# Kernel optimization log

Hardware: AMD Instinct MI355X
Metric: run time of the kernel (lower is better)

## Reference

```python
import jax, jax.numpy as jnp
import numpy as np

T, B, H, L = 512, 64, 512, 2  # seq len, batch, hidden (=input_size), num_layers


def setup_inputs() -> dict:
    key = jax.random.key(0)
    ks = jax.random.split(key, 8)
    s = 1.0 / np.sqrt(H)  # PyTorch LSTMCell init scale
    return {
        "x": jax.random.normal(ks[0], (T, B, H), dtype=jnp.float32),
        "hx": jax.random.normal(ks[1], (L, B, H), dtype=jnp.float32),
        "cx": jax.random.normal(ks[2], (L, B, H), dtype=jnp.float32),
        "W_ih": jax.random.uniform(ks[3], (L, 4 * H, H), jnp.float32, -s, s),
        "W_hh": jax.random.uniform(ks[4], (L, 4 * H, H), jnp.float32, -s, s),
        "b_ih": jax.random.uniform(ks[5], (L, 4 * H), jnp.float32, -s, s),
        "b_hh": jax.random.uniform(ks[6], (L, 4 * H), jnp.float32, -s, s),
    }


def _lstm_cell(x, h, c, W_ih, W_hh, b_ih, b_hh):
    # gates: [B, 4H], PyTorch gate order i, f, g, o
    gates = x @ W_ih.T + b_ih + h @ W_hh.T + b_hh
    i, f, g, o = jnp.split(gates, 4, axis=-1)
    c_new = jax.nn.sigmoid(f) * c + jax.nn.sigmoid(i) * jnp.tanh(g)
    h_new = jax.nn.sigmoid(o) * jnp.tanh(c_new)
    return h_new, c_new


def reference(x, hx, cx, W_ih, W_hh, b_ih, b_hh):
    num_layers = W_ih.shape[0]

    def step(carry, x_t):
        hs, cs = carry  # each [L, B, H]
        inp = x_t
        new_h, new_c = [], []
        for l in range(num_layers):
            h, c = _lstm_cell(inp, hs[l], cs[l], W_ih[l], W_hh[l], b_ih[l], b_hh[l])
            new_h.append(h)
            new_c.append(c)
            inp = h  # feed current-timestep output to next layer (matches torch code)
        return (jnp.stack(new_h), jnp.stack(new_c)), inp

    (hx_f, cx_f), output = jax.lax.scan(step, (hx, cx), x)
    return output, (hx_f, cx_f)
```

## Files before the change

kernel.cpp:

```cpp
#include <hip/hip_runtime.h>
#include <hip/hip_bf16.h>
#include <stdint.h>

#define Tn 512
#define Bn 64
#define Hn 512
#define LDP 520
#define NWG 128
#define NTHR 512
#define BnHn (Bn * Hn)

typedef unsigned short u16;
typedef unsigned int u32;
typedef unsigned long long u64;
typedef __attribute__((ext_vector_type(8))) short bf16x8;
typedef __attribute__((ext_vector_type(4))) float f32x4;

#define HIST_OFF 16384

__device__ __forceinline__ u16 f2bf(float f) {
  u32 u = __float_as_uint(f);
  u = (u + 0x7FFFu + ((u >> 16) & 1u)) >> 16;
  return (u16)u;
}
__device__ __forceinline__ float sigf(float x) { return 1.f / (1.f + __expf(-x)); }
__device__ __forceinline__ float mytanh(float x) {
  float e = __expf(2.f * x);
  return 1.f - 2.f / (e + 1.f);
}
__device__ __forceinline__ u32 ald32(const u32* p) {
  return __hip_atomic_load(p, __ATOMIC_RELAXED, __HIP_MEMORY_SCOPE_AGENT);
}

extern "C" __global__ void __launch_bounds__(256)
lstm_prep(const float* __restrict__ x, const float* __restrict__ hx,
          u32* __restrict__ ws, int xok, int histok) {
  u16* hist = (u16*)((char*)ws + HIST_OFF);
  u16* xbf  = hist + (size_t)(histok ? 513 : 8) * 2 * BnHn;
  const int slot_init = histok ? 512 : 7;
  const int gt = blockIdx.x * 256 + threadIdx.x;
  if (xok) {
#pragma unroll
    for (int i = 0; i < 8; ++i) {
      const int c = gt + (i << 19);
      const float4 v = *(const float4*)(x + (size_t)c * 4);
      const u64 pk = (u64)((u32)f2bf(v.x) | ((u32)f2bf(v.y) << 16)) |
                     ((u64)((u32)f2bf(v.z) | ((u32)f2bf(v.w) << 16)) << 32);
      *(u64*)(xbf + (size_t)c * 4) = pk;
    }
  }
  if (gt < 32768) {
    const int e0 = 2 * gt;
    const int l = e0 >> 15;
    const int off = e0 & 32767;
    const u32 pk = (u32)f2bf(hx[e0]) | ((u32)f2bf(hx[e0 + 1]) << 16);
    *(u32*)(hist + ((size_t)slot_init * 2 + l) * BnHn + off) = pk;
  }
}

extern "C" __global__ void __launch_bounds__(NTHR, 2)
lstm_fused(const float* __restrict__ x, const float* __restrict__ hx,
           const float* __restrict__ cx, const float* __restrict__ Wih,
           const float* __restrict__ Whh, const float* __restrict__ bih,
           const float* __restrict__ bhh, float* __restrict__ out,
           u32* __restrict__ ws, int xok, int histok) {
  __shared__ u16 sh_inp[32 * LDP];
  __shared__ u16 sh_h[32 * LDP];

  __builtin_amdgcn_fence(__ATOMIC_ACQUIRE, "agent");

  const int wg = blockIdx.x;
  const int tid = threadIdx.x;
  const int layer = wg >> 6;
  const int rem = wg & 63;
  const int shalf = rem >> 5;
  const int cc = rem & 31;
  const int wave = tid >> 6;
  const int lane = tid & 63;
  const int l15 = lane & 15;
  const int lhi = lane >> 4;
  const int mt = wave >> 1;
  const int nt = wave & 1;

  u32* flags = ws;
  u16* hist  = (u16*)((char*)ws + HIST_OFF);
  u16* xbf   = hist + (size_t)(histok ? 513 : 8) * 2 * BnHn;
  const int init_slot = histok ? 512 : 7;
  const int gid = layer * 2 + shalf;

  const int jrow = mt * 16 + l15;
  const int gateA = jrow & 3, colA = jrow >> 2;
  const int growA = gateA * Hn + cc * 16 + colA;
  const float* wihp = Wih + ((size_t)layer * 4 * Hn + growA) * Hn;
  const float* whhp = Whh + ((size_t)layer * 4 * Hn + growA) * Hn;
  bf16x8 wih_f[16], whh_f[16];
#pragma unroll
  for (int kt = 0; kt < 16; ++kt) {
    const int k0 = kt * 32 + lhi * 8;
    const float4 va0 = *(const float4*)(wihp + k0);
    const float4 va1 = *(const float4*)(wihp + k0 + 4);
    const float4 vb0 = *(const float4*)(whhp + k0);
    const float4 vb1 = *(const float4*)(whhp + k0 + 4);
    bf16x8 a, b;
    a[0]=(short)f2bf(va0.x); a[1]=(short)f2bf(va0.y); a[2]=(short)f2bf(va0.z); a[3]=(short)f2bf(va0.w);
    a[4]=(short)f2bf(va1.x); a[5]=(short)f2bf(va1.y); a[6]=(short)f2bf(va1.z); a[7]=(short)f2bf(va1.w);
    b[0]=(short)f2bf(vb0.x); b[1]=(short)f2bf(vb0.y); b[2]=(short)f2bf(vb0.z); b[3]=(short)f2bf(vb0.w);
    b[4]=(short)f2bf(vb1.x); b[5]=(short)f2bf(vb1.y); b[6]=(short)f2bf(vb1.z); b[7]=(short)f2bf(vb1.w);
    wih_f[kt] = a; whh_f[kt] = b;
  }

  const int colE = cc * 16 + mt * 4 + lhi;
  const int sampE = shalf * 32 + nt * 16 + l15;
  float bias[4];
#pragma unroll
  for (int r = 0; r < 4; ++r) {
    const int grow = r * Hn + cc * 16 + mt * 4 + lhi;
    bias[r] = bih[layer * 4 * Hn + grow] + bhh[layer * 4 * Hn + grow];
  }
  float c_cur = cx[((size_t)layer * Bn + sampE) * Hn + colE];

  int pidx, tgtoff;
  if (layer == 0) {
    if (lane < 32) { pidx = (0 * 2 + shalf) * 32 + lane; tgtoff = 0; }
    else if (histok) { pidx = (0 * 2 + shalf) * 32 + (lane - 32); tgtoff = 0; }
    else { pidx = (1 * 2 + shalf) * 32 + (lane - 32); tgtoff = 1; }
  } else {
    if (lane < 32) { pidx = (1 * 2 + shalf) * 32 + lane; tgtoff = 0; }
    else { pidx = (0 * 2 + shalf) * 32 + (lane - 32); tgtoff = 1; }
  }
  const u32* pollp = &flags[pidx];

  auto stage_x = [&](int t) {
    if (xok) {
      const u16* ip = xbf + ((size_t)t * Bn + shalf * 32) * Hn;
#pragma unroll
      for (int i = 0; i < 4; ++i) {
        const int chunk = tid + i * 512;
        const int row = chunk >> 6, c0 = (chunk & 63) * 8;
        const uint4 v = *(const uint4*)(ip + (size_t)row * Hn + c0);
        *(uint4*)(&sh_inp[row * LDP + c0]) = v;
      }
    } else {
      const float* xp = x + ((size_t)t * Bn + shalf * 32) * Hn;
#pragma unroll
      for (int i = 0; i < 8; ++i) {
        const int chunk = tid + i * 512;
        const int row = chunk >> 7, c0 = (chunk & 127) * 4;
        const float4 v = *(const float4*)(xp + (size_t)row * Hn + c0);
        const u32 p0 = (u32)f2bf(v.x) | ((u32)f2bf(v.y) << 16);
        const u32 p1 = (u32)f2bf(v.z) | ((u32)f2bf(v.w) << 16);
        *(uint2*)(&sh_inp[row * LDP + c0]) = make_uint2(p0, p1);
      }
    }
  };
  auto stage_h = [&](int slot, int srclayer, u16* dst) {
    const u16* hp = hist + ((size_t)slot * 2 + srclayer) * BnHn + (size_t)(shalf * 32) * Hn;
    if (histok) {
#pragma unroll
      for (int i = 0; i < 4; ++i) {
        const int chunk = tid + i * 512;
        const int row = chunk >> 6, c0 = (chunk & 63) * 8;
        const uint4 v = *(const uint4*)(hp + (size_t)row * Hn + c0);
        *(uint4*)(&dst[row * LDP + c0]) = v;
      }
    } else {
#pragma unroll
      for (int i = 0; i < 8; ++i) {
        const int chunk = tid + i * 512;
        const int row = chunk >> 7, c0 = (chunk & 127) * 4;
        const u64 v = __hip_atomic_load((const u64*)(hp + (size_t)row * Hn + c0),
                                        __ATOMIC_RELAXED, __HIP_MEMORY_SCOPE_AGENT);
        *(u64*)(&dst[row * LDP + c0]) = v;
      }
    }
  };
  f32x4 aI0 = {0.f,0.f,0.f,0.f}, aI1 = {0.f,0.f,0.f,0.f};
  auto compute_aI = [&]() {
    f32x4 t0 = {0.f,0.f,0.f,0.f}, t1 = {0.f,0.f,0.f,0.f};
    const int brow = (nt * 16 + l15) * LDP;
#pragma unroll
    for (int kt = 0; kt < 16; kt += 2) {
      const bf16x8 bi0 = *(const bf16x8*)(&sh_inp[brow + kt * 32 + lhi * 8]);
      const bf16x8 bi1 = *(const bf16x8*)(&sh_inp[brow + (kt + 1) * 32 + lhi * 8]);
      t0 = __builtin_amdgcn_mfma_f32_16x16x32_bf16(wih_f[kt], bi0, t0, 0, 0, 0);
      t1 = __builtin_amdgcn_mfma_f32_16x16x32_bf16(wih_f[kt + 1], bi1, t1, 0, 0, 0);
    }
    aI0 = t0; aI1 = t1;
  };

  if (layer == 0) stage_x(0);
  __syncthreads();
  if (layer == 0) compute_aI();

  const int smax = Tn + 2;
  u32 ep = 0;
  for (int s = 0; s <= smax; ++s) {
    const int t = layer ? s - 3 : s;
    const bool act = (t >= 0) && (t < Tn);

    if (act) {
      const int slotR = (t == 0) ? init_slot : (histok ? (t - 1) : ((t - 1) & 7));
      stage_h(slotR, layer, sh_h);
    }
    __syncthreads();

    float hn = 0.f, cn = 0.f;
    if (act) {
      f32x4 b0 = {0,0,0,0}, b1 = {0,0,0,0};
      const int brow = (nt * 16 + l15) * LDP;
#pragma unroll
      for (int kt = 0; kt < 16; kt += 2) {
        const bf16x8 bh0 = *(const bf16x8*)(&sh_h[brow + kt * 32 + lhi * 8]);
        const bf16x8 bh1 = *(const bf16x8*)(&sh_h[brow + (kt + 1) * 32 + lhi * 8]);
        b0 = __builtin_amdgcn_mfma_f32_16x16x32_bf16(whh_f[kt], bh0, b0, 0, 0, 0);
        b1 = __builtin_amdgcn_mfma_f32_16x16x32_bf16(whh_f[kt + 1], bh1, b1, 0, 0, 0);
      }
      const float gi = aI0[0] + aI1[0] + b0[0] + b1[0] + bias[0];
      const float gf = aI0[1] + aI1[1] + b0[1] + b1[1] + bias[1];
      const float gg = aI0[2] + aI1[2] + b0[2] + b1[2] + bias[2];
      const float go_ = aI0[3] + aI1[3] + b0[3] + b1[3] + bias[3];
      cn = sigf(gf) * c_cur + sigf(gi) * mytanh(gg);
      hn = sigf(go_) * mytanh(cn);
      c_cur = cn;

      const u32 hu = (u32)f2bf(hn);
      const u32 pair = hu | (__shfl_xor(hu, 16) << 16);
      const u32 hi2 = __shfl_xor(pair, 32);
      if (lhi == 0) {
        const int slotW = histok ? t : (t & 7);
        const u64 v8 = (u64)pair | ((u64)hi2 << 32);
        u16* wp = hist + ((size_t)slotW * 2 + layer) * BnHn + (size_t)sampE * Hn + cc * 16 + mt * 4;
        __hip_atomic_store((u64*)wp, v8, __ATOMIC_RELAXED, __HIP_MEMORY_SCOPE_AGENT);
      }
    }
    asm volatile("s_waitcnt vmcnt(0)" ::: "memory");
    __syncthreads();
    ++ep;
    if (tid == 0)
      __hip_atomic_store(&flags[gid * 32 + cc], ep,
                         __ATOMIC_RELAXED, __HIP_MEMORY_SCOPE_AGENT);

    if (act) {
      if (layer == 1)
        out[((size_t)t * Bn + sampE) * Hn + colE] = hn;
      if (t == Tn - 1) {
        out[(size_t)Tn * Bn * Hn + ((size_t)layer * Bn + sampE) * Hn + colE] = hn;
        out[(size_t)Tn * Bn * Hn + (size_t)2 * Bn * Hn + ((size_t)layer * Bn + sampE) * Hn + colE] = cn;
      }
    }
    bool ihnext = false;
    if (layer == 0) {
      if (s + 1 < Tn) { stage_x(s + 1); ihnext = true; }
    } else {
      const int u = s - 2;
      if (u >= 0 && u < Tn) {
        const int slotI = histok ? u : (u & 7);
        stage_h(slotI, 0, sh_inp);
        ihnext = true;
      }
    }
    __syncthreads();
    if (ihnext) compute_aI();

    if (s == smax) break;

    while (true) {
      const u32 v = ald32(pollp);
      if (__all((int)(v + (u32)tgtoff >= ep))) break;
    }
    asm volatile("" ::: "memory");
  }
}

extern "C" void kernel_launch(void* const* d_in, const int* in_sizes, int n_in,
                              void* d_out, int out_size, void* d_ws, size_t ws_size,
                              hipStream_t stream) {
  const float* x   = (const float*)d_in[0];
  const float* hx  = (const float*)d_in[1];
  const float* cx  = (const float*)d_in[2];
  const float* Wih = (const float*)d_in[3];
  const float* Whh = (const float*)d_in[4];
  const float* bih = (const float*)d_in[5];
  const float* bhh = (const float*)d_in[6];
  float* outp = (float*)d_out;
  u32* wsp = (u32*)d_ws;

  const size_t slot_bytes = (size_t)2 * Bn * Hn * 2;
  int histok = (ws_size >= HIST_OFF + (size_t)513 * slot_bytes) ? 1 : 0;
  const size_t xoff = HIST_OFF + (size_t)(histok ? 513 : 8) * slot_bytes;
  int xok = (ws_size >= xoff + (size_t)Tn * Bn * Hn * 2) ? 1 : 0;

  hipMemsetAsync(d_ws, 0, HIST_OFF, stream);

  lstm_prep<<<dim3(2048), dim3(256), 0, stream>>>(x, hx, wsp, xok, histok);

  void* args[] = {(void*)&x, (void*)&hx, (void*)&cx, (void*)&Wih, (void*)&Whh,
                  (void*)&bih, (void*)&bhh, (void*)&outp, (void*)&wsp,
                  (void*)&xok, (void*)&histok};
  hipError_t e = hipLaunchCooperativeKernel((const void*)lstm_fused, dim3(NWG),
                                            dim3(NTHR), args, 0, stream);
  if (e != hipSuccess) {
    lstm_fused<<<dim3(NWG), dim3(NTHR), 0, stream>>>(x, hx, cx, Wih, Whh, bih, bhh,
                                                     outp, wsp, xok, histok);
  }
}
```

Measured before the change: 1.748 ms.

## Replace flag polling with per-element stamped history for LSTM cross-workgroup sync

Adds a stamped mode in which each hidden-state pair is written as a 64-bit word carrying a timestep stamp. Readers spin on the stamps of exactly the data they need instead of waiting on per-workgroup flags, which removes the vmcnt drain, the extra barrier and the flag round-trip on every step. The cost is a history buffer twice as large (about 134MB) that must be memset each call, plus more memory traffic. Launch bounds also drop occupancy from 2 workgroups per CU to 1.

```diff
diff --git a/kernel.cpp b/kernel.cpp
--- a/kernel.cpp
+++ b/kernel.cpp
@@ -17,6 +17,7 @@
 typedef __attribute__((ext_vector_type(4))) float f32x4;
 
 #define HIST_OFF 16384
+#define STAMP_BYTES 134479872ULL
 
 __device__ __forceinline__ u16 f2bf(float f) {
   u32 u = __float_as_uint(f);
@@ -31,13 +32,17 @@
 __device__ __forceinline__ u32 ald32(const u32* p) {
   return __hip_atomic_load(p, __ATOMIC_RELAXED, __HIP_MEMORY_SCOPE_AGENT);
 }
+__device__ __forceinline__ u64 ald64(const u64* p) {
+  return __hip_atomic_load(p, __ATOMIC_RELAXED, __HIP_MEMORY_SCOPE_AGENT);
+}
 
 extern "C" __global__ void __launch_bounds__(256)
 lstm_prep(const float* __restrict__ x, const float* __restrict__ hx,
-          u32* __restrict__ ws, int xok, int histok) {
+          u32* __restrict__ ws, int xok, int smode, int histok) {
   u16* hist = (u16*)((char*)ws + HIST_OFF);
-  u16* xbf  = hist + (size_t)(histok ? 513 : 8) * 2 * BnHn;
-  const int slot_init = histok ? 512 : 7;
+  u64* hstamp = (u64*)((char*)ws + HIST_OFF);
+  u16* xbf = smode ? (u16*)((char*)ws + HIST_OFF + STAMP_BYTES)
+                   : hist + (size_t)(histok ? 513 : 8) * 2 * BnHn;
   const int gt = blockIdx.x * 256 + threadIdx.x;
   if (xok) {
 #pragma unroll
@@ -54,16 +59,24 @@
     const int l = e0 >> 15;
     const int off = e0 & 32767;
     const u32 pk = (u32)f2bf(hx[e0]) | ((u32)f2bf(hx[e0 + 1]) << 16);
-    *(u32*)(hist + ((size_t)slot_init * 2 + l) * BnHn + off) = pk;
-  }
-}
-
-extern "C" __global__ void __launch_bounds__(NTHR, 2)
+    if (smode) {
+      const int b = off >> 9;
+      const int unit = (off & 511) >> 1;
+      hstamp[((size_t)512 * 2 + l) * 16384 + (size_t)b * 256 + unit] =
+          (u64)pk | (15ULL << 32);
+    } else {
+      const int slot_init = histok ? 512 : 7;
+      *(u32*)(hist + ((size_t)slot_init * 2 + l) * BnHn + off) = pk;
+    }
+  }
+}
+
+extern "C" __global__ void __launch_bounds__(NTHR, 1)
 lstm_fused(const float* __restrict__ x, const float* __restrict__ hx,
            const float* __restrict__ cx, const float* __restrict__ Wih,
            const float* __restrict__ Whh, const float* __restrict__ bih,
            const float* __restrict__ bhh, float* __restrict__ out,
-           u32* __restrict__ ws, int xok, int histok) {
+           u32* __restrict__ ws, int xok, int smode, int histok) {
   __shared__ u16 sh_inp[32 * LDP];
   __shared__ u16 sh_h[32 * LDP];
 
@@ -84,7 +97,9 @@
 
   u32* flags = ws;
   u16* hist  = (u16*)((char*)ws + HIST_OFF);
-  u16* xbf   = hist + (size_t)(histok ? 513 : 8) * 2 * BnHn;
+  u64* hstamp = (u64*)((char*)ws + HIST_OFF);
+  u16* xbf = smode ? (u16*)((char*)ws + HIST_OFF + STAMP_BYTES)
+                   : hist + (size_t)(histok ? 513 : 8) * 2 * BnHn;
   const int init_slot = histok ? 512 : 7;
   const int gid = layer * 2 + shalf;
 
@@ -119,6 +134,146 @@
   }
   float c_cur = cx[((size_t)layer * Bn + sampE) * Hn + colE];
 
+  auto stage_x = [&](int t) {
+    if (xok) {
+      const u16* ip = xbf + ((size_t)t * Bn + shalf * 32) * Hn;
+#pragma unroll
+      for (int i = 0; i < 4; ++i) {
+        const int chunk = tid + i * 512;
+        const int row = chunk >> 6, c0 = (chunk & 63) * 8;
+        const uint4 v = *(const uint4*)(ip + (size_t)row * Hn + c0);
+        *(uint4*)(&sh_inp[row * LDP + c0]) = v;
+      }
+    } else {
+      const float* xp = x + ((size_t)t * Bn + shalf * 32) * Hn;
+#pragma unroll
+      for (int i = 0; i < 8; ++i) {
+        const int chunk = tid + i * 512;
+        const int row = chunk >> 7, c0 = (chunk & 127) * 4;
+        const float4 v = *(const float4*)(xp + (size_t)row * Hn + c0);
+        const u32 p0 = (u32)f2bf(v.x) | ((u32)f2bf(v.y) << 16);
+        const u32 p1 = (u32)f2bf(v.z) | ((u32)f2bf(v.w) << 16);
+        *(uint2*)(&sh_inp[row * LDP + c0]) = make_uint2(p0, p1);
+      }
+    }
+  };
+  f32x4 aI0 = {0.f,0.f,0.f,0.f}, aI1 = {0.f,0.f,0.f,0.f};
+  auto compute_aI = [&]() {
+    f32x4 t0 = {0.f,0.f,0.f,0.f}, t1 = {0.f,0.f,0.f,0.f};
+    const int brow = (nt * 16 + l15) * LDP;
+#pragma unroll
+    for (int kt = 0; kt < 16; kt += 2) {
+      const bf16x8 bi0 = *(const bf16x8*)(&sh_inp[brow + kt * 32 + lhi * 8]);
+      const bf16x8 bi1 = *(const bf16x8*)(&sh_inp[brow + (kt + 1) * 32 + lhi * 8]);
+      t0 = __builtin_amdgcn_mfma_f32_16x16x32_bf16(wih_f[kt], bi0, t0, 0, 0, 0);
+      t1 = __builtin_amdgcn_mfma_f32_16x16x32_bf16(wih_f[kt + 1], bi1, t1, 0, 0, 0);
+    }
+    aI0 = t0; aI1 = t1;
+  };
+  auto do_compute = [&](int t, float& hn, float& cn) {
+    f32x4 b0 = {0,0,0,0}, b1 = {0,0,0,0};
+    const int brow = (nt * 16 + l15) * LDP;
+#pragma unroll
+    for (int kt = 0; kt < 16; kt += 2) {
+      const bf16x8 bh0 = *(const bf16x8*)(&sh_h[brow + kt * 32 + lhi * 8]);
+      const bf16x8 bh1 = *(const bf16x8*)(&sh_h[brow + (kt + 1) * 32 + lhi * 8]);
+      b0 = __builtin_amdgcn_mfma_f32_16x16x32_bf16(whh_f[kt], bh0, b0, 0, 0, 0);
+      b1 = __builtin_amdgcn_mfma_f32_16x16x32_bf16(whh_f[kt + 1], bh1, b1, 0, 0, 0);
+    }
+    const float gi = aI0[0] + aI1[0] + b0[0] + b1[0] + bias[0];
+    const float gf = aI0[1] + aI1[1] + b0[1] + b1[1] + bias[1];
+    const float gg = aI0[2] + aI1[2] + b0[2] + b1[2] + bias[2];
+    const float go_ = aI0[3] + aI1[3] + b0[3] + b1[3] + bias[3];
+    cn = sigf(gf) * c_cur + sigf(gi) * mytanh(gg);
+    hn = sigf(go_) * mytanh(cn);
+    c_cur = cn;
+  };
+
+  if (smode) {
+    auto stage_stamped = [&](int slot, int srclayer, u32 expect, u16* dst) {
+      u64* base = hstamp + ((size_t)slot * 2 + srclayer) * 16384 + (size_t)(shalf * 32) * 256;
+#pragma unroll
+      for (int i = 0; i < 8; ++i) {
+        const int p = tid + i * 512;
+        const int samp = p >> 7, up = p & 127;
+        const u64* a = base + samp * 256 + 2 * up;
+        uint4 v = *(const uint4*)a;
+        if (v.y != expect || v.w != expect) {
+          u64 q0, q1;
+          do { q0 = ald64(a); } while ((u32)(q0 >> 32) != expect);
+          do { q1 = ald64(a + 1); } while ((u32)(q1 >> 32) != expect);
+          v.x = (u32)q0; v.z = (u32)q1;
+        }
+        *(uint2*)(&dst[samp * LDP + 4 * up]) = make_uint2(v.x, v.z);
+      }
+    };
+
+    if (layer == 0) stage_x(0);
+    __syncthreads();
+    if (layer == 0) compute_aI();
+
+    const int smax = Tn + 2;
+    for (int s = 0; s <= smax; ++s) {
+      const int t = layer ? s - 3 : s;
+      const bool act = (t >= 0) && (t < Tn);
+
+      if (act) {
+        const int slotR = (t == 0) ? 512 : (t - 1);
+        stage_stamped(slotR, layer, (u32)(t + 15), sh_h);
+      }
+      __syncthreads();
+
+      if (act) {
+        float hn, cn;
+        do_compute(t, hn, cn);
+        const u32 hu = (u32)f2bf(hn);
+        const u32 pair = hu | (__shfl_xor(hu, 16) << 16);
+        if ((lhi & 1) == 0) {
+          const int unit = cc * 8 + mt * 2 + (lhi >> 1);
+          u64* wp = hstamp + ((size_t)t * 2 + layer) * 16384 + (size_t)sampE * 256 + unit;
+          __hip_atomic_store(wp, (u64)pair | ((u64)(u32)(t + 16) << 32),
+                             __ATOMIC_RELAXED, __HIP_MEMORY_SCOPE_AGENT);
+        }
+        if (layer == 1)
+          out[((size_t)t * Bn + sampE) * Hn + colE] = hn;
+        if (t == Tn - 1) {
+          out[(size_t)Tn * Bn * Hn + ((size_t)layer * Bn + sampE) * Hn + colE] = hn;
+          out[(size_t)Tn * Bn * Hn + (size_t)2 * Bn * Hn + ((size_t)layer * Bn + sampE) * Hn + colE] = cn;
+        }
+      }
+      bool ihnext = false;
+      if (layer == 0) {
+        if (s + 1 < Tn) { stage_x(s + 1); ihnext = true; }
+      } else {
+        const int u = s - 2;
+        if (u >= 0 && u < Tn) { stage_stamped(u, 0, (u32)(u + 16), sh_inp); ihnext = true; }
+      }
+      __syncthreads();
+      if (ihnext) compute_aI();
+    }
+    return;
+  }
+
+  auto stage_h = [&](int slot, int srclayer, u16* dst) {
+    const u16* hp = hist + ((size_t)slot * 2 + srclayer) * BnHn + (size_t)(shalf * 32) * Hn;
+    if (histok) {
+#pragma unroll
+      for (int i = 0; i < 4; ++i) {
+        const int chunk = tid + i * 512;
+        const int row = chunk >> 6, c0 = (chunk & 63) * 8;
+        const uint4 v = *(const uint4*)(hp + (size_t)row * Hn + c0);
+        *(uint4*)(&dst[row * LDP + c0]) = v;
+      }
+    } else {
+#pragma unroll
+      for (int i = 0; i < 8; ++i) {
+        const int chunk = tid + i * 512;
+        const int row = chunk >> 7, c0 = (chunk & 127) * 4;
+        const u64 v = ald64((const u64*)(hp + (size_t)row * Hn + c0));
+        *(u64*)(&dst[row * LDP + c0]) = v;
+      }
+    }
+  };
   int pidx, tgtoff;
   if (layer == 0) {
     if (lane < 32) { pidx = (0 * 2 + shalf) * 32 + lane; tgtoff = 0; }
@@ -130,64 +285,6 @@
   }
   const u32* pollp = &flags[pidx];
 
-  auto stage_x = [&](int t) {
-    if (xok) {
-      const u16* ip = xbf + ((size_t)t * Bn + shalf * 32) * Hn;
-#pragma unroll
-      for (int i = 0; i < 4; ++i) {
-        const int chunk = tid + i * 512;
-        const int row = chunk >> 6, c0 = (chunk & 63) * 8;
-        const uint4 v = *(const uint4*)(ip + (size_t)row * Hn + c0);
-        *(uint4*)(&sh_inp[row * LDP + c0]) = v;
-      }
-    } else {
-      const float* xp = x + ((size_t)t * Bn + shalf * 32) * Hn;
-#pragma unroll
-      for (int i = 0; i < 8; ++i) {
-        const int chunk = tid + i * 512;
-        const int row = chunk >> 7, c0 = (chunk & 127) * 4;
-        const float4 v = *(const float4*)(xp + (size_t)row * Hn + c0);
-        const u32 p0 = (u32)f2bf(v.x) | ((u32)f2bf(v.y) << 16);
-        const u32 p1 = (u32)f2bf(v.z) | ((u32)f2bf(v.w) << 16);
-        *(uint2*)(&sh_inp[row * LDP + c0]) = make_uint2(p0, p1);
-      }
-    }
-  };
-  auto stage_h = [&](int slot, int srclayer, u16* dst) {
-    const u16* hp = hist + ((size_t)slot * 2 + srclayer) * BnHn + (size_t)(shalf * 32) * Hn;
-    if (histok) {
-#pragma unroll
-      for (int i = 0; i < 4; ++i) {
-        const int chunk = tid + i * 512;
-        const int row = chunk >> 6, c0 = (chunk & 63) * 8;
-        const uint4 v = *(const uint4*)(hp + (size_t)row * Hn + c0);
-        *(uint4*)(&dst[row * LDP + c0]) = v;
-      }
-    } else {
-#pragma unroll
-      for (int i = 0; i < 8; ++i) {
-        const int chunk = tid + i * 512;
-        const int row = chunk >> 7, c0 = (chunk & 127) * 4;
-        const u64 v = __hip_atomic_load((const u64*)(hp + (size_t)row * Hn + c0),
-                                        __ATOMIC_RELAXED, __HIP_MEMORY_SCOPE_AGENT);
-        *(u64*)(&dst[row * LDP + c0]) = v;
-      }
-    }
-  };
-  f32x4 aI0 = {0.f,0.f,0.f,0.f}, aI1 = {0.f,0.f,0.f,0.f};
-  auto compute_aI = [&]() {
-    f32x4 t0 = {0.f,0.f,0.f,0.f}, t1 = {0.f,0.f,0.f,0.f};
-    const int brow = (nt * 16 + l15) * LDP;
-#pragma unroll
-    for (int kt = 0; kt < 16; kt += 2) {
-      const bf16x8 bi0 = *(const bf16x8*)(&sh_inp[brow + kt * 32 + lhi * 8]);
-      const bf16x8 bi1 = *(const bf16x8*)(&sh_inp[brow + (kt + 1) * 32 + lhi * 8]);
-      t0 = __builtin_amdgcn_mfma_f32_16x16x32_bf16(wih_f[kt], bi0, t0, 0, 0, 0);
-      t1 = __builtin_amdgcn_mfma_f32_16x16x32_bf16(wih_f[kt + 1], bi1, t1, 0, 0, 0);
-    }
-    aI0 = t0; aI1 = t1;
-  };
-
   if (layer == 0) stage_x(0);
   __syncthreads();
   if (layer == 0) compute_aI();
@@ -204,25 +301,9 @@
     }
     __syncthreads();
 
-    float hn = 0.f, cn = 0.f;
     if (act) {
-      f32x4 b0 = {0,0,0,0}, b1 = {0,0,0,0};
-      const int brow = (nt * 16 + l15) * LDP;
-#pragma unroll
-      for (int kt = 0; kt < 16; kt += 2) {
-        const bf16x8 bh0 = *(const bf16x8*)(&sh_h[brow + kt * 32 + lhi * 8]);
-        const bf16x8 bh1 = *(const bf16x8*)(&sh_h[brow + (kt + 1) * 32 + lhi * 8]);
-        b0 = __builtin_amdgcn_mfma_f32_16x16x32_bf16(whh_f[kt], bh0, b0, 0, 0, 0);
-        b1 = __builtin_amdgcn_mfma_f32_16x16x32_bf16(whh_f[kt + 1], bh1, b1, 0, 0, 0);
-      }
-      const float gi = aI0[0] + aI1[0] + b0[0] + b1[0] + bias[0];
-      const float gf = aI0[1] + aI1[1] + b0[1] + b1[1] + bias[1];
-      const float gg = aI0[2] + aI1[2] + b0[2] + b1[2] + bias[2];
-      const float go_ = aI0[3] + aI1[3] + b0[3] + b1[3] + bias[3];
-      cn = sigf(gf) * c_cur + sigf(gi) * mytanh(gg);
-      hn = sigf(go_) * mytanh(cn);
-      c_cur = cn;
-
+      float hn, cn;
+      do_compute(t, hn, cn);
       const u32 hu = (u32)f2bf(hn);
       const u32 pair = hu | (__shfl_xor(hu, 16) << 16);
       const u32 hi2 = __shfl_xor(pair, 32);
@@ -232,6 +313,12 @@
         u16* wp = hist + ((size_t)slotW * 2 + layer) * BnHn + (size_t)sampE * Hn + cc * 16 + mt * 4;
         __hip_atomic_store((u64*)wp, v8, __ATOMIC_RELAXED, __HIP_MEMORY_SCOPE_AGENT);
       }
+      if (layer == 1)
+        out[((size_t)t * Bn + sampE) * Hn + colE] = hn;
+      if (t == Tn - 1) {
+        out[(size_t)Tn * Bn * Hn + ((size_t)layer * Bn + sampE) * Hn + colE] = hn;
+        out[(size_t)Tn * Bn * Hn + (size_t)2 * Bn * Hn + ((size_t)layer * Bn + sampE) * Hn + colE] = cn;
+      }
     }
     asm volatile("s_waitcnt vmcnt(0)" ::: "memory");
     __syncthreads();
@@ -240,14 +327,6 @@
       __hip_atomic_store(&flags[gid * 32 + cc], ep,
                          __ATOMIC_RELAXED, __HIP_MEMORY_SCOPE_AGENT);
 
-    if (act) {
-      if (layer == 1)
-        out[((size_t)t * Bn + sampE) * Hn + colE] = hn;
-      if (t == Tn - 1) {
-        out[(size_t)Tn * Bn * Hn + ((size_t)layer * Bn + sampE) * Hn + colE] = hn;
-        out[(size_t)Tn * Bn * Hn + (size_t)2 * Bn * Hn + ((size_t)layer * Bn + sampE) * Hn + colE] = cn;
-      }
-    }
     bool ihnext = false;
     if (layer == 0) {
       if (s + 1 < Tn) { stage_x(s + 1); ihnext = true; }
@@ -285,22 +364,25 @@
   float* outp = (float*)d_out;
   u32* wsp = (u32*)d_ws;
 
+  const size_t xbytes = (size_t)Tn * Bn * Hn * 2;
+  int smode = (ws_size >= HIST_OFF + STAMP_BYTES + xbytes) ? 1 : 0;
   const size_t slot_bytes = (size_t)2 * Bn * Hn * 2;
   int histok = (ws_size >= HIST_OFF + (size_t)513 * slot_bytes) ? 1 : 0;
-  const size_t xoff = HIST_OFF + (size_t)(histok ? 513 : 8) * slot_bytes;
-  int xok = (ws_size >= xoff + (size_t)Tn * Bn * Hn * 2) ? 1 : 0;
-
-  hipMemsetAsync(d_ws, 0, HIST_OFF, stream);
-
-  lstm_prep<<<dim3(2048), dim3(256), 0, stream>>>(x, hx, wsp, xok, histok);
+  size_t xoff = smode ? (HIST_OFF + STAMP_BYTES)
+                      : (HIST_OFF + (size_t)(histok ? 513 : 8) * slot_bytes);
+  int xok = (ws_size >= xoff + xbytes) ? 1 : 0;
+
+  hipMemsetAsync(d_ws, 0, smode ? (HIST_OFF + STAMP_BYTES) : HIST_OFF, stream);
+
+  lstm_prep<<<dim3(2048), dim3(256), 0, stream>>>(x, hx, wsp, xok, smode, histok);
 
   void* args[] = {(void*)&x, (void*)&hx, (void*)&cx, (void*)&Wih, (void*)&Whh,
                   (void*)&bih, (void*)&bhh, (void*)&outp, (void*)&wsp,
-                  (void*)&xok, (void*)&histok};
+                  (void*)&xok, (void*)&smode, (void*)&histok};
   hipError_t e = hipLaunchCooperativeKernel((const void*)lstm_fused, dim3(NWG),
                                             dim3(NTHR), args, 0, stream);
   if (e != hipSuccess) {
     lstm_fused<<<dim3(NWG), dim3(NTHR), 0, stream>>>(x, hx, cx, Wih, Whh, bih, bhh,
-                                                     outp, wsp, xok, histok);
-  }
-}
+                                                     outp, wsp, xok, smode, histok);
+  }
+}
```

New measurement: 4.389 ms. 2.51x slower.
